# Kernel optimization log

Hardware: AMD Instinct MI355X
Metric: run time of the kernel (lower is better)

Reference implementation:

```python
import jax, jax.numpy as jnp
import numpy as np


def _lstm_scan(x, W, U, b):
    """Unidirectional Keras-style LSTM over x: [B, T, F] -> [B, T, H].
    Gate order (i, f, c, o); sigmoid recurrent activation, tanh activation."""
    B = x.shape[0]
    H = U.shape[0]
    # Precompute input projections for all timesteps: [B, T, 4H]
    xp = jnp.einsum('btf,fg->btg', x, W) + b

    def step(carry, xt):
        h, c = carry
        z = xt + h @ U  # [B, 4H]
        i, f, g, o = jnp.split(z, 4, axis=-1)
        i = jax.nn.sigmoid(i)
        f = jax.nn.sigmoid(f)
        g = jnp.tanh(g)
        o = jax.nn.sigmoid(o)
        c = f * c + i * g
        h = o * jnp.tanh(c)
        return (h, c), h

    init = (jnp.zeros((B, H), x.dtype), jnp.zeros((B, H), x.dtype))
    _, hs = jax.lax.scan(step, init, xp.transpose(1, 0, 2))  # [T, B, H]
    return hs.transpose(1, 0, 2)


def _bidir(x, Wf, Uf, bf, Wb, Ub, bb):
    fwd = _lstm_scan(x, Wf, Uf, bf)
    bwd = jnp.flip(_lstm_scan(jnp.flip(x, axis=1), Wb, Ub, bb), axis=1)
    return jnp.concatenate([fwd, bwd], axis=-1)  # merge_mode='concat'


def setup_inputs() -> dict:
    key = jax.random.key(0)
    ks = jax.random.split(key, 16)
    B, T, F, H = 64, 1024, 64, 256
    s_in0 = 1.0 / np.sqrt(F)
    s_in1 = 1.0 / np.sqrt(2 * H)
    s_rec = 1.0 / np.sqrt(H)
    inp = {
        'x': jax.random.normal(ks[0], (B, T, F), jnp.float32),
        'W0f': jax.random.normal(ks[1], (F, 4 * H), jnp.float32) * s_in0,
        'U0f': jax.random.normal(ks[2], (H, 4 * H), jnp.float32) * s_rec,
        'b0f': jnp.zeros((4 * H,), jnp.float32),
        'W0b': jax.random.normal(ks[3], (F, 4 * H), jnp.float32) * s_in0,
        'U0b': jax.random.normal(ks[4], (H, 4 * H), jnp.float32) * s_rec,
        'b0b': jnp.zeros((4 * H,), jnp.float32),
        'W1f': jax.random.normal(ks[5], (2 * H, 4 * H), jnp.float32) * s_in1,
        'U1f': jax.random.normal(ks[6], (H, 4 * H), jnp.float32) * s_rec,
        'b1f': jnp.zeros((4 * H,), jnp.float32),
        'W1b': jax.random.normal(ks[7], (2 * H, 4 * H), jnp.float32) * s_in1,
        'U1b': jax.random.normal(ks[8], (H, 4 * H), jnp.float32) * s_rec,
        'b1b': jnp.zeros((4 * H,), jnp.float32),
        'Wd': jax.random.normal(ks[9], (2 * H, 1), jnp.float32) * s_in1,
        'bd': jnp.zeros((1,), jnp.float32),
    }
    return inp


def reference(x, W0f, U0f, b0f, W0b, U0b, b0b,
              W1f, U1f, b1f, W1b, U1b, b1b, Wd, bd):
    # Layer 0 bidirectional LSTM -> [B, T, 2H]; dropout is identity at inference
    h = _bidir(x, W0f, U0f, b0f, W0b, U0b, b0b)
    # Layer 1 bidirectional LSTM -> [B, T, 2H]
    h = _bidir(h, W1f, U1f, b1f, W1b, U1b, b1b)
    # Dense(1, linear) head -> [B, T, 1]
    return jnp.einsum('btd,do->bto', h, Wd) + bd
```

## Files before the change

### kernel.cpp

```cpp
#include <hip/hip_runtime.h>
#include <hip/hip_bf16.h>
#include <cstdint>
#include <cstddef>

#define B_ 64
#define T_ 1024

typedef _Float16 half_t;
typedef __attribute__((ext_vector_type(8))) _Float16 half8;
typedef __attribute__((ext_vector_type(4))) float f32x4;
typedef __attribute__((ext_vector_type(8))) unsigned short ushort8;

__device__ __forceinline__ float sigm(float x) { return 1.f / (1.f + __expf(-x)); }
__device__ __forceinline__ float tanh_fast(float x) {
  float e = __expf(2.f * x);
  return 1.f - 2.f / (e + 1.f);
}

__global__ __launch_bounds__(256) void permute_cols(const float* __restrict__ src,
                                                    float* __restrict__ dst, int K) {
  int idx = blockIdx.x * 256 + threadIdx.x;
  if (idx >= K * 1024) return;
  int n = idx & 1023;
  size_t k = (size_t)(idx >> 10);
  dst[idx] = src[(k << 10) + ((size_t)(n & 3) << 8) + (n >> 2)];
}

__global__ __launch_bounds__(256) void pack_u_mfma(const float* __restrict__ src,
                                                   half_t* __restrict__ dst) {
  int tid = blockIdx.x * 256 + threadIdx.x;
  int l = tid & 63;
  int s = (tid >> 6) & 7;
  int n = (tid >> 9) & 1;
  int w = (tid >> 10) & 3;
  int wgc = (tid >> 12) & 7;
  int col = wgc * 128 + w * 32 + n * 16 + (l & 15);
  int hc = col >> 2, g = col & 3;
  int k0 = s * 32 + (l >> 4) * 8;
  half8 v;
#pragma unroll
  for (int j = 0; j < 8; ++j)
    v[j] = (half_t)src[(size_t)(k0 + j) * 1024 + (g << 8) + hc];
  *(half8*)(dst + (size_t)tid * 8) = v;
}

__global__ __launch_bounds__(256) void pack_w0_mfma(const float* __restrict__ src,
                                                    half_t* __restrict__ dst) {
  int line = blockIdx.x * 256 + threadIdx.x;
  int l = line & 63;
  int ks = (line >> 6) & 1;
  int n = (line >> 7) & 1;
  int w = (line >> 8) & 3;
  int wgc = (line >> 10) & 7;
  int col = wgc * 128 + w * 32 + n * 16 + (l & 15);
  int sc = ((col & 3) << 8) + (col >> 2);
  int k0 = ks * 32 + (l >> 4) * 8;
  half8 v;
#pragma unroll
  for (int j = 0; j < 8; ++j)
    v[j] = (half_t)src[(size_t)(k0 + j) * 1024 + sc];
  *(half8*)(dst + (size_t)line * 8) = v;
}

__global__ __launch_bounds__(256) void pack_w1_mfma(const float* __restrict__ src,
                                                    half_t* __restrict__ dst) {
  int tid = blockIdx.x * 256 + threadIdx.x;
  int l = tid & 63;
  int ks = (tid >> 6) & 15;
  int nb = tid >> 10;
  int colp = nb * 16 + (l & 15);
  int sc = ((colp & 3) << 8) + (colp >> 2);
  int k0 = ks * 32 + (l >> 4) * 8;
  half8 v;
#pragma unroll
  for (int j = 0; j < 8; ++j)
    v[j] = (half_t)src[(size_t)(k0 + j) * 1024 + sc];
  *(half8*)(dst + (size_t)tid * 8) = v;
}

__global__ __launch_bounds__(256) void pack_x_f16(const float* __restrict__ x,
                                                  unsigned short* __restrict__ xi) {
  int idx = blockIdx.x * 256 + threadIdx.x;
  int b = idx & 15;
  int q = (idx >> 4) & 3;
  int ks = (idx >> 6) & 1;
  int t = (idx >> 7) & 1023;
  int bg = idx >> 17;
  const float* src = x + ((size_t)(bg * 16 + b) * T_ + t) * 64 + ks * 32 + q * 8;
  ushort8 v;
#pragma unroll
  for (int j = 0; j < 8; ++j) {
    half_t h = (half_t)src[j];
    v[j] = __builtin_bit_cast(unsigned short, h);
  }
  *(ushort8*)(xi + (size_t)idx * 8) = v;
}

__global__ __launch_bounds__(256) void init_out(float* __restrict__ out,
                                                const float* __restrict__ bd, int n) {
  int i = blockIdx.x * 256 + threadIdx.x;
  if (i < n) out[i] = bd[0];
}

__global__ __launch_bounds__(256) void diag_out(float* __restrict__ out, int n, float v) {
  int i = blockIdx.x * 256 + threadIdx.x;
  if (i < n) out[i] = (i == 0) ? v : 0.f;
}

__global__ __launch_bounds__(256) void proj1_mfma(
    const unsigned short* __restrict__ h0,
    const half_t* __restrict__ Wf, const half_t* __restrict__ Wb,
    const float* __restrict__ bpf, const float* __restrict__ bpb,
    float* __restrict__ xp, int s0, int Tc) {
  const int dir = blockIdx.z;
  const half_t* Wpk = dir ? Wb : Wf;
  const float* bs = dir ? bpb : bpf;
  const int b = blockIdx.y;
  const int mt = blockIdx.x;
  const int tid = threadIdx.x;
  const int l = tid & 63, w = tid >> 6;

  __shared__ __align__(16) unsigned short A_lds[16][520];

  {
    int r = tid >> 4, c16 = tid & 15;
    int sl = mt * 16 + r;
    int t = dir ? (T_ - 1 - s0 - sl) : (s0 + sl);
    const ushort8* srcp =
        (const ushort8*)(h0 + ((size_t)b * T_ + t) * 512 + c16 * 32);
#pragma unroll
    for (int u = 0; u < 4; ++u)
      *(ushort8*)&A_lds[r][c16 * 32 + u * 8] = __builtin_nontemporal_load(srcp + u);
  }
  __syncthreads();

  f32x4 acc[16];
#pragma unroll
  for (int n = 0; n < 16; ++n) acc[n] = (f32x4){0.f, 0.f, 0.f, 0.f};

  for (int ks = 0; ks < 16; ++ks) {
    half8 a = *(const half8*)&A_lds[l & 15][ks * 32 + (l >> 4) * 8];
    const half_t* bp_ = Wpk + (((size_t)(w * 16) * 16 + ks) * 64 + l) * 8;
#pragma unroll
    for (int n = 0; n < 16; ++n) {
      half8 bfr = *(const half8*)(bp_ + (size_t)n * 16 * 64 * 8);
      acc[n] = __builtin_amdgcn_mfma_f32_16x16x32_f16(a, bfr, acc[n], 0, 0, 0);
    }
  }

#pragma unroll
  for (int n = 0; n < 16; ++n) {
    int col = (w * 16 + n) * 16 + (l & 15);
    float bias = bs[col];
#pragma unroll
    for (int r = 0; r < 4; ++r) {
      int sl = mt * 16 + (l >> 4) * 4 + r;
      __builtin_nontemporal_store(
          acc[n][r] + bias,
          &xp[(((size_t)dir * B_ + b) * Tc + sl) * 1024 + col]);
    }
  }
}

template <int L0>
__global__ __launch_bounds__(256, 1) void lstm_scan_mfma(
    const float* __restrict__ xp,
    const unsigned short* __restrict__ xi,
    const half_t* __restrict__ W0f_, const half_t* __restrict__ W0b_,
    const float* __restrict__ b0f_, const float* __restrict__ b0b_,
    const half_t* __restrict__ Upk_f, const half_t* __restrict__ Upk_b,
    float* __restrict__ carry_c,
    unsigned* __restrict__ payl, unsigned* __restrict__ flagw,
    int s0, int Tc, int tagbase,
    unsigned short* __restrict__ hout,
    const float* __restrict__ Wd, float* __restrict__ out) {
  const int blk = blockIdx.x;
  const int unit = blk & 7;
  const int wgc = blk >> 3;
  const int dir = unit & 1;
  const int bg = unit >> 1;
  const int b0u = bg * 16;
  const int tid = threadIdx.x;
  const int l = tid & 63;
  const int w = tid >> 6;

  __shared__ __align__(16) unsigned short A_lds[4096];
  __shared__ __align__(16) unsigned short hstage[512];
  __shared__ float red_sm[64];

  const half_t* Upk = dir ? Upk_b : Upk_f;
  half8 U[2][8];
  {
    const half_t* up = Upk + (size_t)(wgc * 4 + w) * 8192;
#pragma unroll
    for (int n = 0; n < 2; ++n)
#pragma unroll
      for (int s = 0; s < 8; ++s)
        U[n][s] = *(const half8*)(up + ((size_t)(n * 8 + s) * 64 + l) * 8);
  }

  const int b_lane = 4 * (l >> 4) + (l & 3);
  const int hcb = wgc * 32 + w * 8 + ((l >> 2) & 3);
  const int colb = wgc * 128 + w * 32 + (l & 15);
  float cst[2];
#pragma unroll
  for (int n = 0; n < 2; ++n)
    cst[n] = (s0 == 0) ? 0.f
        : carry_c[((size_t)dir * B_ + b0u + b_lane) * 256 + hcb + n * 4];

  float wdl[2] = {0.f, 0.f};
  half8 W0r[2][2];
  float bias0[2] = {0.f, 0.f};
  const unsigned short* xib = nullptr;
  if (L0) {
    const half_t* W0pk = dir ? W0b_ : W0f_;
    const float* bs0 = dir ? b0b_ : b0f_;
#pragma unroll
    for (int n = 0; n < 2; ++n) {
      bias0[n] = bs0[colb + n * 16];
#pragma unroll
      for (int ks = 0; ks < 2; ++ks)
        W0r[n][ks] = *(const half8*)(W0pk +
            ((size_t)(((wgc * 4 + w) * 2 + n) * 2 + ks) * 64 + l) * 8);
    }
    xib = xi + (size_t)bg * T_ * 1024;
  } else {
    wdl[0] = Wd[dir * 256 + hcb];
    wdl[1] = Wd[dir * 256 + hcb + 4];
  }

  unsigned* payl_u = payl + (size_t)unit * 4096;
  unsigned* flag_u = flagw + unit * 16;

  if (s0 == 0) {
#pragma unroll
    for (int i = 0; i < 8; ++i) ((unsigned*)A_lds)[tid * 8 + i] = 0u;
  } else {
    unsigned dd[8];
#pragma unroll
    for (int i = 0; i < 8; ++i)
      dd[i] = __hip_atomic_load(payl_u + 2048 + tid * 8 + i,
                                __ATOMIC_RELAXED, __HIP_MEMORY_SCOPE_AGENT);
#pragma unroll
    for (int i = 0; i < 8; ++i)
      ((unsigned*)A_lds)[tid * 8 + i] = dd[i];
  }
  __syncthreads();

  const float* xpu = L0 ? nullptr : (xp + (size_t)(dir * B_ + b0u) * Tc * 1024);

  float xpre[2][4];
  half8 xfre[2];
  {
    if (L0) {
      int t0f = dir ? (T_ - 1 - s0) : s0;
#pragma unroll
      for (int ks = 0; ks < 2; ++ks)
        xfre[ks] = __builtin_nontemporal_load(
            (const half8*)((const half_t*)xib + (size_t)t0f * 1024 +
                           ((ks * 4 + (l >> 4)) * 16 + (l & 15)) * 8));
    } else {
#pragma unroll
      for (int n = 0; n < 2; ++n)
#pragma unroll
        for (int r = 0; r < 4; ++r)
          xpre[n][r] = __builtin_nontemporal_load(
              &xpu[((size_t)(4 * (l >> 4) + r) * Tc) * 1024 + colb + n * 16]);
    }
  }

  const int hbl = (w * 16 + b_lane) * 8 + ((l >> 2) & 3);

  for (int sl = 0; sl < Tc; ++sl) {
    const int s = s0 + sl;
    const int t = dir ? (T_ - 1 - s) : s;
    const int slot = s & 1;

    f32x4 acc[2];
    if (L0) {
#pragma unroll
      for (int n = 0; n < 2; ++n)
#pragma unroll
        for (int r = 0; r < 4; ++r) acc[n][r] = bias0[n];
      half8 xa0 = xfre[0], xa1 = xfre[1];
#pragma unroll
      for (int n = 0; n < 2; ++n) {
        acc[n] = __builtin_amdgcn_mfma_f32_16x16x32_f16(xa0, W0r[n][0], acc[n], 0, 0, 0);
        acc[n] = __builtin_amdgcn_mfma_f32_16x16x32_f16(xa1, W0r[n][1], acc[n], 0, 0, 0);
      }
    } else {
#pragma unroll
      for (int n = 0; n < 2; ++n)
#pragma unroll
        for (int r = 0; r < 4; ++r) acc[n][r] = xpre[n][r];
    }

    half8 a[8];
#pragma unroll
    for (int sK = 0; sK < 8; ++sK)
      a[sK] = *(const half8*)&((const half_t*)A_lds)[((sK * 4 + (l >> 4)) * 16 + (l & 15)) * 8];

#pragma unroll
    for (int sK = 0; sK < 8; ++sK) {
      acc[0] = __builtin_amdgcn_mfma_f32_16x16x32_f16(a[sK], U[0][sK], acc[0], 0, 0, 0);
      acc[1] = __builtin_amdgcn_mfma_f32_16x16x32_f16(a[sK], U[1][sK], acc[1], 0, 0, 0);
    }

    float vhead = 0.f;
    unsigned short hu2[2];
#pragma unroll
    for (int n = 0; n < 2; ++n) {
      float v0 = acc[n][0], v1 = acc[n][1], v2 = acc[n][2], v3 = acc[n][3];
      float x0 = __shfl_xor(v1, 1), x1 = __shfl_xor(v0, 1);
      float x2 = __shfl_xor(v3, 1), x3 = __shfl_xor(v2, 1);
      float a0 = (l & 1) ? x0 : v0;
      float a1 = (l & 1) ? v1 : x1;
      float a2 = (l & 1) ? x2 : v2;
      float a3 = (l & 1) ? v3 : x3;
      float y0 = __shfl_xor(a2, 2), y1 = __shfl_xor(a3, 2);
      float y2 = __shfl_xor(a0, 2), y3 = __shfl_xor(a1, 2);
      float u0 = (l & 2) ? y0 : a0;
      float u1 = (l & 2) ? y1 : a1;
      float u2 = (l & 2) ? a2 : y2;
      float u3 = (l & 2) ? a3 : y3;

      float iG = sigm(u0), fG = sigm(u1), gG = tanh_fast(u2), oG = sigm(u3);
      float cn = fG * cst[n] + iG * gG;
      cst[n] = cn;
      float h = oG * tanh_fast(cn);

      if (!L0) vhead += h * wdl[n];
      hu2[n] = __builtin_bit_cast(unsigned short, (half_t)h);
      if (sl == Tc - 1)
        carry_c[((size_t)dir * B_ + b0u + b_lane) * 256 + hcb + n * 4] = cn;
    }
    hstage[hbl] = hu2[0];
    hstage[hbl + 4] = hu2[1];
    if (!L0) {
      vhead += __shfl_xor(vhead, 4);
      vhead += __shfl_xor(vhead, 8);
      if ((l & 12) == 0) red_sm[w * 16 + b_lane] = vhead;
    }
    __syncthreads();

    const unsigned* hs32 = (const unsigned*)hstage;
    __hip_atomic_store(payl_u + slot * 2048 + wgc * 256 + tid, hs32[tid],
                       __ATOMIC_RELAXED, __HIP_MEMORY_SCOPE_AGENT);

    asm volatile("s_waitcnt vmcnt(0)" ::: "memory");
    __syncthreads();
    const unsigned want = (unsigned)(tagbase + s + 1);
    if (tid == 0)
      __hip_atomic_store(flag_u + slot * 8 + wgc, want,
                         __ATOMIC_RELAXED, __HIP_MEMORY_SCOPE_AGENT);

    if (L0) {
      int bb = tid >> 4, cc = tid & 15;
      __builtin_nontemporal_store(
          hs32[(cc >> 2) * 64 + bb * 4 + (cc & 3)],
          (unsigned*)hout + ((size_t)(b0u + bb) * T_ + t) * 256 + dir * 128 +
              wgc * 16 + cc);
    } else if (tid < 16) {
      atomicAdd(out + (((size_t)(b0u + tid)) << 10) + t,
                (red_sm[tid] + red_sm[16 + tid]) +
                (red_sm[32 + tid] + red_sm[48 + tid]));
    }

    if (sl + 1 < Tc) {
      if (L0) {
        int tn = dir ? (T_ - 2 - s) : (s + 1);
#pragma unroll
        for (int ks = 0; ks < 2; ++ks)
          xfre[ks] = __builtin_nontemporal_load(
              (const half8*)((const half_t*)xib + (size_t)tn * 1024 +
                             ((ks * 4 + (l >> 4)) * 16 + (l & 15)) * 8));
      } else {
#pragma unroll
        for (int n = 0; n < 2; ++n)
#pragma unroll
          for (int r = 0; r < 4; ++r)
            xpre[n][r] = __builtin_nontemporal_load(
                &xpu[((size_t)(4 * (l >> 4) + r) * Tc + sl + 1) * 1024 + colb + n * 16]);
      }

      if (tid < 8 && tid != wgc) {
        while (__hip_atomic_load(flag_u + slot * 8 + tid, __ATOMIC_RELAXED,
                                 __HIP_MEMORY_SCOPE_AGENT) != want) {}
      }
      __syncthreads();
      unsigned dd[8];
      const int g = tid >> 5;
      if (g == wgc) {
#pragma unroll
        for (int i = 0; i < 8; ++i) dd[i] = hs32[(tid & 31) * 8 + i];
      } else {
#pragma unroll
        for (int i = 0; i < 8; ++i)
          dd[i] = __hip_atomic_load(payl_u + slot * 2048 + tid * 8 + i,
                                    __ATOMIC_RELAXED, __HIP_MEMORY_SCOPE_AGENT);
      }
#pragma unroll
      for (int i = 0; i < 8; ++i)
        ((unsigned*)A_lds)[tid * 8 + i] = dd[i];
      __syncthreads();
    }
  }
}

extern "C" void kernel_launch(void* const* d_in, const int* in_sizes, int n_in,
                              void* d_out, int out_size, void* d_ws, size_t ws_size,
                              hipStream_t stream) {
  const float* x   = (const float*)d_in[0];
  const float* W0f = (const float*)d_in[1];
  const float* U0f = (const float*)d_in[2];
  const float* b0f = (const float*)d_in[3];
  const float* W0b = (const float*)d_in[4];
  const float* U0b = (const float*)d_in[5];
  const float* b0b = (const float*)d_in[6];
  const float* W1f = (const float*)d_in[7];
  const float* U1f = (const float*)d_in[8];
  const float* b1f = (const float*)d_in[9];
  const float* W1b = (const float*)d_in[10];
  const float* U1b = (const float*)d_in[11];
  const float* b1b = (const float*)d_in[12];
  const float* Wd  = (const float*)d_in[13];
  const float* bd  = (const float*)d_in[14];
  float* out = (float*)d_out;
  char* ws = (char*)d_ws;

  const size_t H0_BYTES   = (size_t)B_ * T_ * 512 * 2;
  const size_t UPK_BYTES  = (size_t)262144 * 2;
  const size_t W0PK_BYTES = (size_t)8192 * 8 * 2;
  const size_t W1PK_BYTES = (size_t)512 * 1024 * 2;
  const size_t XI_BYTES   = (size_t)B_ * T_ * 64 * 2;
  const size_t BP_BYTES   = 1024 * 4;
  const size_t CC_BYTES   = (size_t)2 * B_ * 256 * 4;
  const size_t PL_BYTES   = (size_t)8 * 4096 * 4;
  const size_t FL_BYTES   = 1024;
  const size_t REPACK = 4 * UPK_BYTES + 2 * W0PK_BYTES + 2 * W1PK_BYTES +
                        XI_BYTES + 4 * BP_BYTES + CC_BYTES + PL_BYTES +
                        FL_BYTES + 1024;

  int Tc = 0;
  for (int tc = 256; tc >= 64; tc >>= 1) {
    size_t xpb = (size_t)2 * B_ * tc * 1024 * 4;
    if (H0_BYTES + REPACK + xpb <= ws_size) { Tc = tc; break; }
  }
  if (!Tc) {
    float v = 1000.f + (float)(ws_size >> 20);
    diag_out<<<(out_size + 255) / 256, 256, 0, stream>>>(out, out_size, v);
    return;
  }

  size_t off = 0;
  unsigned short* h0 = (unsigned short*)(ws + off); off += H0_BYTES;
  half_t* Up00 = (half_t*)(ws + off); off += UPK_BYTES;
  half_t* Up01 = (half_t*)(ws + off); off += UPK_BYTES;
  half_t* Up10 = (half_t*)(ws + off); off += UPK_BYTES;
  half_t* Up11 = (half_t*)(ws + off); off += UPK_BYTES;
  half_t* W0pf = (half_t*)(ws + off); off += W0PK_BYTES;
  half_t* W0pb = (half_t*)(ws + off); off += W0PK_BYTES;
  half_t* W1pf = (half_t*)(ws + off); off += W1PK_BYTES;
  half_t* W1pb = (half_t*)(ws + off); off += W1PK_BYTES;
  unsigned short* xi = (unsigned short*)(ws + off); off += XI_BYTES;
  float* bp0f = (float*)(ws + off); off += BP_BYTES;
  float* bp0b = (float*)(ws + off); off += BP_BYTES;
  float* bp1f = (float*)(ws + off); off += BP_BYTES;
  float* bp1b = (float*)(ws + off); off += BP_BYTES;
  float* carry_c = (float*)(ws + off); off += CC_BYTES;
  unsigned* payl = (unsigned*)(ws + off); off += PL_BYTES;
  unsigned* flagw = (unsigned*)(ws + off); off += FL_BYTES;
  off = (off + 255) & ~(size_t)255;
  float* xpc = (float*)(ws + off);

  pack_u_mfma<<<128, 256, 0, stream>>>(U0f, Up00);
  pack_u_mfma<<<128, 256, 0, stream>>>(U0b, Up01);
  pack_u_mfma<<<128, 256, 0, stream>>>(U1f, Up10);
  pack_u_mfma<<<128, 256, 0, stream>>>(U1b, Up11);
  pack_w0_mfma<<<32, 256, 0, stream>>>(W0f, W0pf);
  pack_w0_mfma<<<32, 256, 0, stream>>>(W0b, W0pb);
  pack_w1_mfma<<<256, 256, 0, stream>>>(W1f, W1pf);
  pack_w1_mfma<<<256, 256, 0, stream>>>(W1b, W1pb);
  pack_x_f16<<<2048, 256, 0, stream>>>(x, xi);
  permute_cols<<<4, 256, 0, stream>>>(b0f, bp0f, 1);
  permute_cols<<<4, 256, 0, stream>>>(b0b, bp0b, 1);
  permute_cols<<<4, 256, 0, stream>>>(b1f, bp1f, 1);
  permute_cols<<<4, 256, 0, stream>>>(b1b, bp1b, 1);

  lstm_scan_mfma<1><<<64, 256, 0, stream>>>(
      nullptr, xi, W0pf, W0pb, bp0f, bp0b, Up00, Up01, carry_c,
      payl, flagw, 0, T_, 0, h0, nullptr, nullptr);

  init_out<<<(out_size + 255) / 256, 256, 0, stream>>>(out, bd, out_size);
  const int nch = T_ / Tc;
  const dim3 pgrid(Tc / 16, B_, 2);
  for (int ci = 0; ci < nch; ++ci) {
    int s0c = ci * Tc;
    proj1_mfma<<<pgrid, 256, 0, stream>>>(h0, W1pf, W1pb, bp1f, bp1b,
                                          xpc, s0c, Tc);
    lstm_scan_mfma<0><<<64, 256, 0, stream>>>(
        xpc, nullptr, nullptr, nullptr, nullptr, nullptr, Up10, Up11, carry_c,
        payl, flagw, s0c, Tc, 1024, nullptr, Wd, out);
  }
}
```

Before: 6.581 ms.

## Merge pairs of LSTM scan workgroups into 512-thread blocks to halve cross-block sync

Each recurrent scan unit now uses 4 workgroups of 512 threads instead of 8 of 256. Each block covers two of the old column slices, so half of the h exchange stays in LDS and each step spin-waits on 3 peer flags instead of 7. The cost is more waves per CU, a higher register-pressure bound under the 512-thread launch bound, and heavier per-block barriers, while the total number of CUs busy on the serial recurrence drops.

```diff
diff --git a/kernel.cpp b/kernel.cpp
--- a/kernel.cpp
+++ b/kernel.cpp
@@ -163,7 +163,7 @@
 }
 
 template <int L0>
-__global__ __launch_bounds__(256, 1) void lstm_scan_mfma(
+__global__ __launch_bounds__(512, 1) void lstm_scan_mfma(
     const float* __restrict__ xp,
     const unsigned short* __restrict__ xi,
     const half_t* __restrict__ W0f_, const half_t* __restrict__ W0b_,
@@ -182,16 +182,18 @@
   const int b0u = bg * 16;
   const int tid = threadIdx.x;
   const int l = tid & 63;
-  const int w = tid >> 6;
+  const int w8 = tid >> 6;
+  const int wgco = wgc * 2 + (w8 >> 2);
+  const int w = w8 & 3;
 
   __shared__ __align__(16) unsigned short A_lds[4096];
-  __shared__ __align__(16) unsigned short hstage[512];
-  __shared__ float red_sm[64];
+  __shared__ __align__(16) unsigned short hstage[1024];
+  __shared__ float red_sm[128];
 
   const half_t* Upk = dir ? Upk_b : Upk_f;
   half8 U[2][8];
   {
-    const half_t* up = Upk + (size_t)(wgc * 4 + w) * 8192;
+    const half_t* up = Upk + (size_t)(wgco * 4 + w) * 8192;
 #pragma unroll
     for (int n = 0; n < 2; ++n)
 #pragma unroll
@@ -200,8 +202,8 @@
   }
 
   const int b_lane = 4 * (l >> 4) + (l & 3);
-  const int hcb = wgc * 32 + w * 8 + ((l >> 2) & 3);
-  const int colb = wgc * 128 + w * 32 + (l & 15);
+  const int hcb = wgco * 32 + w * 8 + ((l >> 2) & 3);
+  const int colb = wgco * 128 + w * 32 + (l & 15);
   float cst[2];
 #pragma unroll
   for (int n = 0; n < 2; ++n)
@@ -221,7 +223,7 @@
 #pragma unroll
       for (int ks = 0; ks < 2; ++ks)
         W0r[n][ks] = *(const half8*)(W0pk +
-            ((size_t)(((wgc * 4 + w) * 2 + n) * 2 + ks) * 64 + l) * 8);
+            ((size_t)(((wgco * 4 + w) * 2 + n) * 2 + ks) * 64 + l) * 8);
     }
     xib = xi + (size_t)bg * T_ * 1024;
   } else {
@@ -234,16 +236,16 @@
 
   if (s0 == 0) {
 #pragma unroll
-    for (int i = 0; i < 8; ++i) ((unsigned*)A_lds)[tid * 8 + i] = 0u;
+    for (int i = 0; i < 4; ++i) ((unsigned*)A_lds)[tid * 4 + i] = 0u;
   } else {
-    unsigned dd[8];
-#pragma unroll
-    for (int i = 0; i < 8; ++i)
-      dd[i] = __hip_atomic_load(payl_u + 2048 + tid * 8 + i,
+    unsigned dd[4];
+#pragma unroll
+    for (int i = 0; i < 4; ++i)
+      dd[i] = __hip_atomic_load(payl_u + 2048 + tid * 4 + i,
                                 __ATOMIC_RELAXED, __HIP_MEMORY_SCOPE_AGENT);
 #pragma unroll
-    for (int i = 0; i < 8; ++i)
-      ((unsigned*)A_lds)[tid * 8 + i] = dd[i];
+    for (int i = 0; i < 4; ++i)
+      ((unsigned*)A_lds)[tid * 4 + i] = dd[i];
   }
   __syncthreads();
 
@@ -269,7 +271,7 @@
     }
   }
 
-  const int hbl = (w * 16 + b_lane) * 8 + ((l >> 2) & 3);
+  const int hbl = (w8 >> 2) * 512 + (w * 16 + b_lane) * 8 + ((l >> 2) & 3);
 
   for (int sl = 0; sl < Tc; ++sl) {
     const int s = s0 + sl;
@@ -339,12 +341,12 @@
     if (!L0) {
       vhead += __shfl_xor(vhead, 4);
       vhead += __shfl_xor(vhead, 8);
-      if ((l & 12) == 0) red_sm[w * 16 + b_lane] = vhead;
+      if ((l & 12) == 0) red_sm[w8 * 16 + b_lane] = vhead;
     }
     __syncthreads();
 
     const unsigned* hs32 = (const unsigned*)hstage;
-    __hip_atomic_store(payl_u + slot * 2048 + wgc * 256 + tid, hs32[tid],
+    __hip_atomic_store(payl_u + slot * 2048 + wgc * 512 + tid, hs32[tid],
                        __ATOMIC_RELAXED, __HIP_MEMORY_SCOPE_AGENT);
 
     asm volatile("s_waitcnt vmcnt(0)" ::: "memory");
@@ -355,15 +357,18 @@
                          __ATOMIC_RELAXED, __HIP_MEMORY_SCOPE_AGENT);
 
     if (L0) {
-      int bb = tid >> 4, cc = tid & 15;
+      int sub = tid >> 8, r = tid & 255;
+      int bb = r >> 4, cc = r & 15;
       __builtin_nontemporal_store(
-          hs32[(cc >> 2) * 64 + bb * 4 + (cc & 3)],
+          hs32[sub * 256 + (cc >> 2) * 64 + bb * 4 + (cc & 3)],
           (unsigned*)hout + ((size_t)(b0u + bb) * T_ + t) * 256 + dir * 128 +
-              wgc * 16 + cc);
+              (wgc * 2 + sub) * 16 + cc);
     } else if (tid < 16) {
-      atomicAdd(out + (((size_t)(b0u + tid)) << 10) + t,
-                (red_sm[tid] + red_sm[16 + tid]) +
-                (red_sm[32 + tid] + red_sm[48 + tid]));
+      float sum = ((red_sm[tid] + red_sm[16 + tid]) +
+                   (red_sm[32 + tid] + red_sm[48 + tid])) +
+                  ((red_sm[64 + tid] + red_sm[80 + tid]) +
+                   (red_sm[96 + tid] + red_sm[112 + tid]));
+      atomicAdd(out + (((size_t)(b0u + tid)) << 10) + t, sum);
     }
 
     if (sl + 1 < Tc) {
@@ -383,25 +388,26 @@
                 &xpu[((size_t)(4 * (l >> 4) + r) * Tc + sl + 1) * 1024 + colb + n * 16]);
       }
 
-      if (tid < 8 && tid != wgc) {
+      if (tid < 4 && tid != wgc) {
         while (__hip_atomic_load(flag_u + slot * 8 + tid, __ATOMIC_RELAXED,
                                  __HIP_MEMORY_SCOPE_AGENT) != want) {}
       }
       __syncthreads();
-      unsigned dd[8];
-      const int g = tid >> 5;
-      if (g == wgc) {
-#pragma unroll
-        for (int i = 0; i < 8; ++i) dd[i] = hs32[(tid & 31) * 8 + i];
+      unsigned dd[4];
+      const int g = tid >> 6;
+      if ((g >> 1) == wgc) {
+#pragma unroll
+        for (int i = 0; i < 4; ++i)
+          dd[i] = hs32[(g & 1) * 256 + (tid & 63) * 4 + i];
       } else {
 #pragma unroll
-        for (int i = 0; i < 8; ++i)
-          dd[i] = __hip_atomic_load(payl_u + slot * 2048 + tid * 8 + i,
+        for (int i = 0; i < 4; ++i)
+          dd[i] = __hip_atomic_load(payl_u + slot * 2048 + tid * 4 + i,
                                     __ATOMIC_RELAXED, __HIP_MEMORY_SCOPE_AGENT);
       }
 #pragma unroll
-      for (int i = 0; i < 8; ++i)
-        ((unsigned*)A_lds)[tid * 8 + i] = dd[i];
+      for (int i = 0; i < 4; ++i)
+        ((unsigned*)A_lds)[tid * 4 + i] = dd[i];
       __syncthreads();
     }
   }
@@ -487,7 +493,7 @@
   permute_cols<<<4, 256, 0, stream>>>(b1f, bp1f, 1);
   permute_cols<<<4, 256, 0, stream>>>(b1b, bp1b, 1);
 
-  lstm_scan_mfma<1><<<64, 256, 0, stream>>>(
+  lstm_scan_mfma<1><<<32, 512, 0, stream>>>(
       nullptr, xi, W0pf, W0pb, bp0f, bp0b, Up00, Up01, carry_c,
       payl, flagw, 0, T_, 0, h0, nullptr, nullptr);
 
@@ -498,7 +504,7 @@
     int s0c = ci * Tc;
     proj1_mfma<<<pgrid, 256, 0, stream>>>(h0, W1pf, W1pb, bp1f, bp1b,
                                           xpc, s0c, Tc);
-    lstm_scan_mfma<0><<<64, 256, 0, stream>>>(
+    lstm_scan_mfma<0><<<32, 512, 0, stream>>>(
         xpc, nullptr, nullptr, nullptr, nullptr, nullptr, Up10, Up11, carry_c,
         payl, flagw, s0c, Tc, 1024, nullptr, Wd, out);
   }
```

Result: faster. 6.438 ms (-2.2%).
